# Performance work log

Hardware: AMD Instinct MI355X
Metric: run time of the kernel (lower is better)

Reference implementation:

```python
import jax, jax.numpy as jnp
import numpy as np

HEADS = 6
FILTERS = (16, 32, 64)
V_FEATS = 11
N_NODES = 30000
N_EDGES = 480000


def setup_inputs() -> dict:
    key = jax.random.key(0)
    ks = jax.random.split(key, 20)
    d = {}
    d["x_int"] = jax.random.normal(ks[0], (N_NODES, V_FEATS), jnp.float32)
    d["x_nh"] = jax.random.normal(ks[1], (N_NODES, V_FEATS), jnp.float32)
    d["ei_int"] = jax.random.randint(ks[2], (2, N_EDGES), 0, N_NODES, jnp.int32)
    d["ei_nh"] = jax.random.randint(ks[3], (2, N_EDGES), 0, N_NODES, jnp.int32)
    f_in = V_FEATS
    kidx = 4
    for i, f in enumerate(FILTERS, 1):
        s = 1.0 / np.sqrt(f_in)
        d[f"W{i}"] = (jax.random.normal(ks[kidx], (f_in, HEADS * f), jnp.float32) * s); kidx += 1
        sa = 1.0 / np.sqrt(f)
        d[f"a{i}s"] = (jax.random.normal(ks[kidx], (HEADS, f), jnp.float32) * sa); kidx += 1
        d[f"a{i}d"] = (jax.random.normal(ks[kidx], (HEADS, f), jnp.float32) * sa); kidx += 1
        f_in = HEADS * f
    d["Wd"] = jax.random.normal(ks[kidx], (2 * HEADS * FILTERS[-1], 1), jnp.float32) * 0.05
    d["bd"] = jnp.zeros((1,), jnp.float32)
    return d


def _gat_layer(h, src, dst, W, a_s, a_d):
    """One multi-head graph-attention (DGAT) layer, heads concatenated.
    h: [N, F_in]; W: [F_in, H*F_out]; a_s, a_d: [H, F_out]."""
    N = h.shape[0]
    H, Fo = a_s.shape
    z = (h @ W).reshape(N, H, Fo)                      # [N, H, Fo]
    e_src = jnp.einsum('nhf,hf->nh', z, a_s)           # [N, H]
    e_dst = jnp.einsum('nhf,hf->nh', z, a_d)
    e = jax.nn.leaky_relu(e_src[src] + e_dst[dst], 0.2)  # [E, H]
    # softmax over incoming edges of each destination node
    e_max = jax.ops.segment_max(e, dst, num_segments=N)  # [N, H] (-inf for empty)
    ex = jnp.exp(e - e_max[dst])
    denom = jax.ops.segment_sum(ex, dst, num_segments=N)
    alpha = ex / (denom[dst] + 1e-16)                   # [E, H]
    msg = z[src] * alpha[:, :, None]                    # [E, H, Fo]
    out = jax.ops.segment_sum(msg, dst, num_segments=N) # [N, H, Fo]
    return jax.nn.elu(out).reshape(N, H * Fo)


def reference(x_int, x_nh, W1, a1s, a1d, W2, a2s, a2d, W3, a3s, a3d, Wd, bd, ei_int, ei_nh):
    layers = [(W1, a1s, a1d), (W2, a2s, a2d), (W3, a3s, a3d)]

    def run(h, ei):
        src, dst = ei[0], ei[1]
        for (W, a_s, a_d) in layers:
            h = _gat_layer(h, src, dst, W, a_s, a_d)
        return h

    hi = run(x_int, ei_int)   # [N, 384]
    hn = run(x_nh, ei_nh)     # [N, 384]
    x = jnp.concatenate([hi, hn], axis=1)       # [N, 768]
    x = jnp.sum(x, axis=0).reshape(1, -1)       # [1, 768] sum pooling
    norm = jnp.maximum(jnp.linalg.norm(x, axis=1, keepdims=True), 1e-12)
    x = x / norm                                # F.normalize
    x = x @ Wd + bd                             # Dense, linear nonlin
    return jnp.squeeze(x, 1)                    # [1]
```

## Files before the change

### kernel.cpp

```cpp
#include <hip/hip_runtime.h>
#include <math.h>

#define N_NODES 30000
#define N_EDGES 480000
#define HEADS   6
#define NN2 (2 * N_NODES)
#define NE2 (2 * N_EDGES)

typedef __attribute__((ext_vector_type(8))) short bf16x8;
typedef __attribute__((ext_vector_type(4))) float f32x4;
typedef __attribute__((ext_vector_type(2))) float f32x2;
typedef __attribute__((ext_vector_type(4))) unsigned u32x4;

__device__ __forceinline__ unsigned short f2bf(float f) {
    unsigned u = __float_as_uint(f);
    u += 0x7fffu + ((u >> 16) & 1u);
    return (unsigned short)(u >> 16);
}

__global__ void gemm1_es_kernel(const float* __restrict__ x0, const float* __restrict__ x1,
                                const float* __restrict__ W, const float* __restrict__ a_s,
                                const float* __restrict__ a_d,
                                unsigned char* __restrict__ zf8b, float* __restrict__ es8,
                                float* __restrict__ ed8) {
    constexpr int K = 11, HF = 96, TM = 16, Fo = 16;
    __shared__ float hs[TM * K];
    const int m0 = blockIdx.x * TM;
    const float* h = (m0 < N_NODES) ? (x0 + (size_t)m0 * K)
                                    : (x1 + (size_t)(m0 - N_NODES) * K);
    const int j = blockIdx.y * 64 + threadIdx.x;
    for (int idx = threadIdx.x; idx < TM * K; idx += 64) hs[idx] = h[idx];
    __syncthreads();
    if (j >= HF) return;
    float acc[TM];
#pragma unroll
    for (int m = 0; m < TM; ++m) acc[m] = 0.f;
    for (int k = 0; k < K; ++k) {
        float w = W[k * HF + j];
#pragma unroll
        for (int m = 0; m < TM; ++m) acc[m] = fmaf(hs[m * K + k], w, acc[m]);
    }
    const float as_v = a_s[j];
    const float ad_v = a_d[j];
    const int hh = j >> 4;
    const int fo = j & 15;
#pragma unroll
    for (int m = 0; m < TM; ++m) {
        const int pk = __builtin_amdgcn_cvt_pk_fp8_f32(acc[m], acc[m], 0, false);
        zf8b[((size_t)hh * NN2 + (m0 + m)) * Fo + fo] = (unsigned char)pk;
    }
#pragma unroll
    for (int m = 0; m < TM; ++m) {
        float ep = acc[m] * as_v;
        float dp = acc[m] * ad_v;
#pragma unroll
        for (int d = 1; d < 16; d <<= 1) {
            ep += __shfl_xor(ep, d);
            dp += __shfl_xor(dp, d);
        }
        if ((threadIdx.x & 15) == 0) {
            es8[(size_t)(m0 + m) * 8 + hh] = ep;
            ed8[(size_t)(m0 + m) * 8 + hh] = dp;
        }
    }
}

__global__ void convert_wt_kernel(const float* __restrict__ W, unsigned short* __restrict__ Wt,
                                  int K, int HF) {
    const int idx = blockIdx.x * 256 + threadIdx.x;
    if (idx >= K * HF) return;
    const int k = idx / HF;
    const int n = idx - k * HF;
    Wt[n * K + k] = f2bf(W[idx]);
}

template <int K, int HF>
__global__ __launch_bounds__(256) void gemm_es_kernel(
        const unsigned short* __restrict__ hbf, const unsigned short* __restrict__ Wt,
        const float* __restrict__ a_s, const float* __restrict__ a_d,
        unsigned char* __restrict__ zf8b, float* __restrict__ es8,
        float* __restrict__ ed8) {
    constexpr int KSTEPS = K / 32;
    constexpr int Fo  = HF / HEADS;
    constexpr int TPH = Fo / 16;
    constexpr int NT  = HF / 16;
    constexpr int PAD = 8;
    constexpr int LROW = K + PAD;
    constexpr int NCH = 16 * K / 8;
    __shared__ unsigned short bl[16 * LROW];

    const int tid  = threadIdx.x;
    const int wid  = blockIdx.x * 4 + (tid >> 6);
    const bool active = wid < NN2 / 16;
    const int lane = tid & 63;
    const int r16  = lane & 15;
    const int quad = lane >> 4;
    const int m0 = active ? wid * 16 : 0;

    bf16x8 afrag[KSTEPS];
    const unsigned short* ap = hbf + (size_t)(m0 + r16) * K + quad * 8;
#pragma unroll
    for (int i = 0; i < KSTEPS; ++i) afrag[i] = *(const bf16x8*)(ap + i * 32);

    u32x4 st[2];
#pragma unroll
    for (int j = 0; j < 2; ++j) {
        const int c = tid + j * 256;
        if (c < NCH) st[j] = *(const u32x4*)(Wt + (size_t)c * 8);
    }

    float es_p[4] = {0.f, 0.f, 0.f, 0.f};
    float ed_p[4] = {0.f, 0.f, 0.f, 0.f};
    for (int t = 0; t < NT; ++t) {
        __syncthreads();
#pragma unroll
        for (int j = 0; j < 2; ++j) {
            const int c = tid + j * 256;
            if (c < NCH) {
                const int row = c / (K / 8);
                const int co  = c - row * (K / 8);
                *(u32x4*)(bl + row * LROW + co * 8) = st[j];
            }
        }
        if (t + 1 < NT) {
            const unsigned short* wp = Wt + (size_t)(t + 1) * 16 * K;
#pragma unroll
            for (int j = 0; j < 2; ++j) {
                const int c = tid + j * 256;
                if (c < NCH) st[j] = *(const u32x4*)(wp + (size_t)c * 8);
            }
        }
        __syncthreads();

        f32x4 acc = {0.f, 0.f, 0.f, 0.f};
        const unsigned short* bp = bl + r16 * LROW + quad * 8;
#pragma unroll
        for (int i = 0; i < KSTEPS; ++i) {
            const bf16x8 bfrag = *(const bf16x8*)(bp + i * 32);
            acc = __builtin_amdgcn_mfma_f32_16x16x32_bf16(afrag[i], bfrag, acc, 0, 0, 0);
        }
        const float as_v = a_s[t * 16 + r16];
        const float ad_v = a_d[t * 16 + r16];
        const int th = t / TPH;
        const int fo = (t % TPH) * 16 + r16;
        unsigned char* zp = zf8b + ((size_t)th * NN2 + (m0 + quad * 4)) * Fo + fo;
#pragma unroll
        for (int r = 0; r < 4; ++r) {
            const int pk = __builtin_amdgcn_cvt_pk_fp8_f32(acc[r], acc[r], 0, false);
            if (active) zp[(size_t)r * Fo] = (unsigned char)pk;
            es_p[r] = fmaf(acc[r], as_v, es_p[r]);
            ed_p[r] = fmaf(acc[r], ad_v, ed_p[r]);
        }
        if (((t + 1) % TPH) == 0) {
            const int h = t / TPH;
#pragma unroll
            for (int r = 0; r < 4; ++r) {
                float ep = es_p[r], dp = ed_p[r];
#pragma unroll
                for (int d = 1; d < 16; d <<= 1) {
                    ep += __shfl_xor(ep, d);
                    dp += __shfl_xor(dp, d);
                }
                if (active && r16 == 0) {
                    es8[(size_t)(m0 + quad * 4 + r) * 8 + h] = ep;
                    ed8[(size_t)(m0 + quad * 4 + r) * 8 + h] = dp;
                }
                es_p[r] = 0.f;
                ed_p[r] = 0.f;
            }
        }
    }
}

__global__ void zero_int_kernel(int* __restrict__ p, int n) {
    const int i = blockIdx.x * 256 + threadIdx.x;
    if (i < n) p[i] = 0;
}

__global__ void hist2_kernel(const int* __restrict__ ei0, const int* __restrict__ ei1,
                             int* __restrict__ cnt) {
    const int e = blockIdx.x * 256 + threadIdx.x;
    if (e >= NE2) return;
    const int g = e >= N_EDGES;
    const int* ei = g ? ei1 : ei0;
    const int e2 = e - g * N_EDGES;
    atomicAdd(&cnt[g * N_NODES + ei[N_EDGES + e2]], 1);
}

#define SCAN_NB ((NN2 + 1023) / 1024)
__global__ void scan1_kernel(int* tmp, int* __restrict__ bsum) {
    __shared__ int s[1024];
    const int t = threadIdx.x;
    const int gid = blockIdx.x * 1024 + t;
    const int v = (gid < NN2) ? tmp[gid] : 0;
    s[t] = v;
    __syncthreads();
    for (int d = 1; d < 1024; d <<= 1) {
        int x = (t >= d) ? s[t - d] : 0;
        __syncthreads();
        s[t] += x;
        __syncthreads();
    }
    tmp[gid] = s[t] - v;
    if (t == 1023) bsum[blockIdx.x] = s[1023];
}

__global__ void scan2_kernel(int* __restrict__ bsum, int* __restrict__ boff) {
    if (threadIdx.x == 0) {
        int a = 0;
        for (int i = 0; i < SCAN_NB; ++i) { boff[i] = a; a += bsum[i]; }
        boff[SCAN_NB] = a;
    }
}

__global__ void scan3_kernel(int* tmp, const int* __restrict__ boff,
                             int* __restrict__ off) {
    const int gid = blockIdx.x * 1024 + threadIdx.x;
    if (gid < NN2) {
        const int o = tmp[gid] + boff[gid >> 10];
        off[gid] = o;
        tmp[gid] = o;
    }
    if (gid == 0) off[NN2] = boff[SCAN_NB];
}

__global__ void scatter2_kernel(const int* __restrict__ ei0, const int* __restrict__ ei1,
                                int* __restrict__ cursor,
                                unsigned* __restrict__ csrp) {
    const int e = blockIdx.x * 256 + threadIdx.x;
    if (e >= NE2) return;
    const int g = e >= N_EDGES;
    const int* ei = g ? ei1 : ei0;
    const int e2 = e - g * N_EDGES;
    const int src = g * N_NODES + ei[e2];
    const int dst = g * N_NODES + ei[N_EDGES + e2];
    const int slot = atomicAdd(&cursor[dst], 1);
    csrp[slot] = ((unsigned)dst << 16) | (unsigned)src;
}

__global__ __launch_bounds__(256) void edgew_kernel(
        const unsigned* __restrict__ csrp,
        const float* __restrict__ es8, const float* __restrict__ ed8,
        unsigned* __restrict__ pA, unsigned* __restrict__ pB) {
    const int s = blockIdx.x * 256 + threadIdx.x;
    if (s >= NE2) return;
    const unsigned sd = csrp[s];
    const unsigned src = sd & 0xFFFFu;
    const unsigned dst = sd >> 16;
    const f32x4 ea = *(const f32x4*)(es8 + src * 8u);
    const f32x2 eb = *(const f32x2*)(es8 + src * 8u + 4);
    const f32x4 da = *(const f32x4*)(ed8 + dst * 8u);
    const f32x2 db = *(const f32x2*)(ed8 + dst * 8u + 4);
    float ev[6];
    ev[0] = ea.x + da.x; ev[1] = ea.y + da.y; ev[2] = ea.z + da.z;
    ev[3] = ea.w + da.w; ev[4] = eb.x + db.x; ev[5] = eb.y + db.y;
#pragma unroll
    for (int h = 0; h < 6; ++h) {
        float v = ev[h];
        v = fmaxf(v, 0.2f * v);
        const unsigned rec = ((unsigned)f2bf(__expf(v)) << 16) | src;
        unsigned* p = (h < 3) ? (pA + (size_t)h * NE2) : (pB + (size_t)(h - 3) * NE2);
        p[s] = rec;
    }
}

template <int HF, int GS, int MAIN, int G>
__global__ __launch_bounds__(256) void agg_sub_kernel(
        const int* __restrict__ off, const unsigned* __restrict__ ewA,
        const unsigned* __restrict__ ewB,
        const unsigned* __restrict__ zf8, unsigned short* __restrict__ outz) {
    constexpr int Fo  = HF / HEADS;
    constexpr int L   = Fo / 4;
    constexpr int EPI = GS / L;
    constexpr int GPW = 64 / GS;
    constexpr int NB  = 4 * GPW;
    constexpr int BPH = NN2 / NB;
    int h, blk;
    {
        const int r = blockIdx.x & 7, g = blockIdx.x >> 3;
        if (r < 6) {
            if (g >= MAIN) return;
            h = r; blk = g;
        } else {
            const int k = (r - 6) * G + g;
            if (k >= 6 * (BPH - MAIN)) return;
            h = k % 6; blk = MAIN + k / 6;
        }
    }
    const int wavid = threadIdx.x >> 6;
    const int lane  = threadIdx.x & 63;
    const int grp = lane / GS;
    const int lg  = lane - grp * GS;
    const int eo = lg / L;
    const int fp = lg - eo * L;
    const int n = blk * NB + wavid * GPW + grp;

    const int s0  = off[n];
    const int deg = off[n + 1] - s0;
    const unsigned* ewp = ((h < 3) ? (ewA + (size_t)h * NE2)
                                   : (ewB + (size_t)(h - 3) * NE2)) + s0;
    const unsigned* zh = zf8 + (size_t)h * ((size_t)NN2 * L);

    float a0 = 0.f, a1 = 0.f, a2 = 0.f, a3 = 0.f, lsum = 0.f;
    for (int ib = 0; ib < deg; ib += 4 * EPI) {
        unsigned rec[4];
#pragma unroll
        for (int k = 0; k < 4; ++k) {
            const int idx = ib + k * EPI + eo;
            rec[k] = ewp[idx < deg ? idx : 0];
        }
        unsigned zz[4];
#pragma unroll
        for (int k = 0; k < 4; ++k)
            zz[k] = zh[(rec[k] & 0xFFFFu) * (unsigned)L + (unsigned)fp];
#pragma unroll
        for (int k = 0; k < 4; ++k) {
            const int idx = ib + k * EPI + eo;
            float ww = __uint_as_float(rec[k] & 0xFFFF0000u);
            ww = (idx < deg) ? ww : 0.f;
            lsum += ww;
            const f32x2 lo = __builtin_amdgcn_cvt_pk_f32_fp8((int)zz[k], false);
            const f32x2 hi = __builtin_amdgcn_cvt_pk_f32_fp8((int)zz[k], true);
            a0 = fmaf(ww, lo.x, a0);
            a1 = fmaf(ww, lo.y, a1);
            a2 = fmaf(ww, hi.x, a2);
            a3 = fmaf(ww, hi.y, a3);
        }
    }
#pragma unroll
    for (int d = L; d < GS; d <<= 1) {
        a0 += __shfl_xor(a0, d);
        a1 += __shfl_xor(a1, d);
        a2 += __shfl_xor(a2, d);
        a3 += __shfl_xor(a3, d);
        lsum += __shfl_xor(lsum, d);
    }
    if (eo == 0) {
        const float inv = 1.f / (lsum + 1e-16f);
        float o0 = a0 * inv, o1 = a1 * inv, o2 = a2 * inv, o3 = a3 * inv;
        o0 = o0 > 0.f ? o0 : (__expf(o0) - 1.f);
        o1 = o1 > 0.f ? o1 : (__expf(o1) - 1.f);
        o2 = o2 > 0.f ? o2 : (__expf(o2) - 1.f);
        o3 = o3 > 0.f ? o3 : (__expf(o3) - 1.f);
        unsigned short* op = outz + (size_t)n * HF + h * Fo + 4 * fp;
        *(unsigned*)op       = (unsigned)f2bf(o0) | ((unsigned)f2bf(o1) << 16);
        *(unsigned*)(op + 2) = (unsigned)f2bf(o2) | ((unsigned)f2bf(o3) << 16);
    }
}

#define POOL_BLOCKS 3072
#define POOL_WAVES 2048
__global__ __launch_bounds__(256) void agg_pool_kernel(
        const int* __restrict__ off, const unsigned* __restrict__ ewA,
        const unsigned* __restrict__ ewB,
        const unsigned* __restrict__ zf8, float* __restrict__ pooled) {
    __shared__ float lds[128];
    int h, slot;
    {
        const int r = blockIdx.x & 7, g = blockIdx.x >> 3;
        if (r < 6) { h = r; slot = g; }
        else { h = g % 6; slot = 384 + (r - 6) * 64 + g / 6; }
    }
    const int wavid = threadIdx.x >> 6;
    const int ws    = slot * 4 + wavid;
    const int lane  = threadIdx.x & 63;
    const int c  = lane >> 2;
    const int fp = lane & 3;
    const unsigned* ewh = (h < 3) ? (ewA + (size_t)h * NE2)
                                  : (ewB + (size_t)(h - 3) * NE2);
    const u32x4* zq = (const u32x4*)(zf8 + (size_t)h * ((size_t)NN2 * 16));

    if (threadIdx.x < 128) lds[threadIdx.x] = 0.f;
    __syncthreads();

    float p0[16], p1[16];
#pragma unroll
    for (int j = 0; j < 16; ++j) { p0[j] = 0.f; p1[j] = 0.f; }

    for (int base = ws * 16; base < NN2; base += POOL_WAVES * 16) {
        const int n = base + c;
        const bool valid = n < NN2;
        int s0 = 0, deg = 0;
        if (valid) { s0 = off[n]; deg = off[n + 1] - s0; }
        int dmx = deg;
#pragma unroll
        for (int d = 4; d < 64; d <<= 1) {
            const int o = __shfl_xor(dmx, d);
            dmx = o > dmx ? o : dmx;
        }
        const unsigned* ewp = ewh + s0;
        float acc[16];
#pragma unroll
        for (int j = 0; j < 16; ++j) acc[j] = 0.f;
        float lsum = 0.f;
        for (int ib = 0; ib < dmx; ib += 4) {
            unsigned rec[4];
#pragma unroll
            for (int k = 0; k < 4; ++k) {
                const int idx = ib + k;
                rec[k] = ewp[idx < deg ? idx : 0];
            }
            u32x4 zz[4];
#pragma unroll
            for (int k = 0; k < 4; ++k)
                zz[k] = zq[(rec[k] & 0xFFFFu) * 4u + (unsigned)fp];
#pragma unroll
            for (int k = 0; k < 4; ++k) {
                float w = __uint_as_float(rec[k] & 0xFFFF0000u);
                w = ((ib + k) < deg) ? w : 0.f;
                lsum += w;
#pragma unroll
                for (int d = 0; d < 4; ++d) {
                    const f32x2 lo = __builtin_amdgcn_cvt_pk_f32_fp8((int)zz[k][d], false);
                    const f32x2 hi = __builtin_amdgcn_cvt_pk_f32_fp8((int)zz[k][d], true);
                    acc[4 * d + 0] = fmaf(w, lo.x, acc[4 * d + 0]);
                    acc[4 * d + 1] = fmaf(w, lo.y, acc[4 * d + 1]);
                    acc[4 * d + 2] = fmaf(w, hi.x, acc[4 * d + 2]);
                    acc[4 * d + 3] = fmaf(w, hi.y, acc[4 * d + 3]);
                }
            }
        }
        if (valid) {
            const float inv = 1.f / (lsum + 1e-16f);
            if (base < N_NODES) {
#pragma unroll
                for (int j = 0; j < 16; ++j) {
                    float o = acc[j] * inv;
                    o = o > 0.f ? o : (__expf(o) - 1.f);
                    p0[j] += o;
                }
            } else {
#pragma unroll
                for (int j = 0; j < 16; ++j) {
                    float o = acc[j] * inv;
                    o = o > 0.f ? o : (__expf(o) - 1.f);
                    p1[j] += o;
                }
            }
        }
    }
#pragma unroll
    for (int d = 4; d < 64; d <<= 1) {
#pragma unroll
        for (int j = 0; j < 16; ++j) {
            p0[j] += __shfl_xor(p0[j], d);
            p1[j] += __shfl_xor(p1[j], d);
        }
    }
    if (lane < 4) {
#pragma unroll
        for (int j = 0; j < 16; ++j) {
            atomicAdd(&lds[fp * 16 + j], p0[j]);
            atomicAdd(&lds[64 + fp * 16 + j], p1[j]);
        }
    }
    __syncthreads();
    if (threadIdx.x < 128) {
        const int g2 = threadIdx.x >> 6;
        const int f  = threadIdx.x & 63;
        atomicAdd(&pooled[g2 * 384 + h * 64 + f], lds[threadIdx.x]);
    }
}

__global__ void zero_pooled_kernel(float* __restrict__ p) {
    const int i = blockIdx.x * 256 + threadIdx.x;
    if (i < 768) p[i] = 0.f;
}

__global__ void final_kernel(const float* __restrict__ pooled, const float* __restrict__ Wd,
                             const float* __restrict__ bd, float* __restrict__ outp) {
    __shared__ float s_ss[256], s_dot[256];
    const int t = threadIdx.x;
    float ss = 0.f, dot = 0.f;
    for (int c = t; c < 768; c += 256) {
        const float v = pooled[c];
        ss  = fmaf(v, v, ss);
        dot = fmaf(v, Wd[c], dot);
    }
    s_ss[t] = ss; s_dot[t] = dot;
    __syncthreads();
    for (int off = 128; off > 0; off >>= 1) {
        if (t < off) { s_ss[t] += s_ss[t + off]; s_dot[t] += s_dot[t + off]; }
        __syncthreads();
    }
    if (t == 0) {
        const float norm = fmaxf(sqrtf(s_ss[0]), 1e-12f);
        outp[0] = s_dot[0] / norm + bd[0];
    }
}

extern "C" void kernel_launch(void* const* d_in, const int* in_sizes, int n_in,
                              void* d_out, int out_size, void* d_ws, size_t ws_size,
                              hipStream_t stream) {
    const float* x_int = (const float*)d_in[0];
    const float* x_nh  = (const float*)d_in[1];
    const int*   ei_int = (const int*)d_in[2];
    const int*   ei_nh  = (const int*)d_in[3];
    const float* W1  = (const float*)d_in[4];
    const float* a1s = (const float*)d_in[5];
    const float* a1d = (const float*)d_in[6];
    const float* W2  = (const float*)d_in[7];
    const float* a2s = (const float*)d_in[8];
    const float* a2d = (const float*)d_in[9];
    const float* W3  = (const float*)d_in[10];
    const float* a3s = (const float*)d_in[11];
    const float* a3d = (const float*)d_in[12];
    const float* Wd  = (const float*)d_in[13];
    const float* bd  = (const float*)d_in[14];
    float* out = (float*)d_out;

    unsigned short* hbf_a = (unsigned short*)d_ws;
    unsigned short* hbf_b = hbf_a + (size_t)NN2 * 96;
    unsigned short* wt2   = hbf_b + (size_t)NN2 * 192;
    unsigned short* wt3   = wt2   + (size_t)96 * 192;
    unsigned* zf8 = (unsigned*)(wt3 + (size_t)192 * 384);
    float* es8   = (float*)(zf8 + (size_t)NN2 * 96);
    float* ed8   = es8 + (size_t)NN2 * 8;
    float* pooled = ed8 + (size_t)NN2 * 8;
    int* tmp     = (int*)(pooled + 768);
    int* bsum    = tmp + SCAN_NB * 1024;
    int* boff    = bsum + SCAN_NB;
    int* off     = boff + SCAN_NB + 1;
    unsigned* csrp = (unsigned*)(off + NN2 + 1);
    unsigned char* zf8b = (unsigned char*)zf8;

    unsigned* ew13A = (unsigned*)hbf_b;
    unsigned* ew13B = ew13A + (size_t)3 * NE2;
    unsigned* ew2A  = (unsigned*)hbf_a;
    unsigned* ew2B  = zf8 + (size_t)NN2 * 48;

    zero_pooled_kernel<<<3, 256, 0, stream>>>(pooled);
    convert_wt_kernel<<<(96 * 192 + 255) / 256, 256, 0, stream>>>(W2, wt2, 96, 192);
    convert_wt_kernel<<<(192 * 384 + 255) / 256, 256, 0, stream>>>(W3, wt3, 192, 384);

    zero_int_kernel<<<(NN2 + 255) / 256, 256, 0, stream>>>(tmp, NN2);
    hist2_kernel<<<(NE2 + 255) / 256, 256, 0, stream>>>(ei_int, ei_nh, tmp);
    scan1_kernel<<<SCAN_NB, 1024, 0, stream>>>(tmp, bsum);
    scan2_kernel<<<1, 64, 0, stream>>>(bsum, boff);
    scan3_kernel<<<SCAN_NB, 1024, 0, stream>>>(tmp, boff, off);
    scatter2_kernel<<<(NE2 + 255) / 256, 256, 0, stream>>>(ei_int, ei_nh, tmp, csrp);

    const int mfma_blocks = (NN2 / 16 + 3) / 4;
    const int ew_blocks = (NE2 + 255) / 256;

    gemm1_es_kernel<<<dim3(NN2 / 16, 2), 64, 0, stream>>>(x_int, x_nh, W1, a1s, a1d, zf8b,
                                                          es8, ed8);
    edgew_kernel<<<ew_blocks, 256, 0, stream>>>(csrp, es8, ed8, ew13A, ew13B);
    agg_sub_kernel<96, 16, 2812, 2814><<<8 * 2814, 256, 0, stream>>>(off, ew13A, ew13B,
                                                                     zf8, hbf_a);
    gemm_es_kernel<96, 192><<<mfma_blocks, 256, 0, stream>>>(hbf_a, wt2, a2s, a2d, zf8b,
                                                             es8, ed8);
    edgew_kernel<<<ew_blocks, 256, 0, stream>>>(csrp, es8, ed8, ew2A, ew2B);
    agg_sub_kernel<192, 32, 5625, 5625><<<45000, 256, 0, stream>>>(off, ew2A, ew2B,
                                                                   zf8, hbf_b);
    gemm_es_kernel<192, 384><<<mfma_blocks, 256, 0, stream>>>(hbf_b, wt3, a3s, a3d, zf8b,
                                                              es8, ed8);
    edgew_kernel<<<ew_blocks, 256, 0, stream>>>(csrp, es8, ed8, ew13A, ew13B);
    agg_pool_kernel<<<POOL_BLOCKS, 256, 0, stream>>>(off, ew13A, ew13B, zf8, pooled);

    final_kernel<<<1, 256, 0, stream>>>(pooled, Wd, bd, out);
}
```

Before: 492.1 us.

## Sort nodes by in-degree so aggregation waves process similar-degree nodes

```diff
diff --git a/kernel.cpp b/kernel.cpp
--- a/kernel.cpp
+++ b/kernel.cpp
@@ -236,6 +236,39 @@
     const int dst = g * N_NODES + ei[N_EDGES + e2];
     const int slot = atomicAdd(&cursor[dst], 1);
     csrp[slot] = ((unsigned)dst << 16) | (unsigned)src;
+}
+
+__global__ void deghist_kernel(const int* __restrict__ off, int* __restrict__ dbuk) {
+    const int n = blockIdx.x * 256 + threadIdx.x;
+    if (n >= NN2) return;
+    const int deg = off[n + 1] - off[n];
+    const int b = deg < 511 ? deg : 511;
+    atomicAdd(&dbuk[(n >= N_NODES) * 512 + b], 1);
+}
+
+__global__ void degscan_kernel(int* __restrict__ dbuk) {
+    __shared__ int s[1024];
+    const int t = threadIdx.x;
+    const int v = dbuk[t];
+    s[t] = v;
+    __syncthreads();
+    for (int d = 1; d < 1024; d <<= 1) {
+        int x = (t >= d) ? s[t - d] : 0;
+        __syncthreads();
+        s[t] += x;
+        __syncthreads();
+    }
+    dbuk[t] = s[t] - v;
+}
+
+__global__ void degscatter_kernel(const int* __restrict__ off, int* __restrict__ dbuk,
+                                  unsigned short* __restrict__ sorted) {
+    const int n = blockIdx.x * 256 + threadIdx.x;
+    if (n >= NN2) return;
+    const int deg = off[n + 1] - off[n];
+    const int b = deg < 511 ? deg : 511;
+    const int pos = atomicAdd(&dbuk[(n >= N_NODES) * 512 + b], 1);
+    sorted[pos] = (unsigned short)n;
 }
 
 __global__ __launch_bounds__(256) void edgew_kernel(
@@ -266,8 +299,8 @@
 
 template <int HF, int GS, int MAIN, int G>
 __global__ __launch_bounds__(256) void agg_sub_kernel(
-        const int* __restrict__ off, const unsigned* __restrict__ ewA,
-        const unsigned* __restrict__ ewB,
+        const int* __restrict__ off, const unsigned short* __restrict__ sorted,
+        const unsigned* __restrict__ ewA, const unsigned* __restrict__ ewB,
         const unsigned* __restrict__ zf8, unsigned short* __restrict__ outz) {
     constexpr int Fo  = HF / HEADS;
     constexpr int L   = Fo / 4;
@@ -293,7 +326,8 @@
     const int lg  = lane - grp * GS;
     const int eo = lg / L;
     const int fp = lg - eo * L;
-    const int n = blk * NB + wavid * GPW + grp;
+    const int npos = blk * NB + wavid * GPW + grp;
+    const int n = sorted[npos];
 
     const int s0  = off[n];
     const int deg = off[n + 1] - s0;
@@ -351,8 +385,8 @@
 #define POOL_BLOCKS 3072
 #define POOL_WAVES 2048
 __global__ __launch_bounds__(256) void agg_pool_kernel(
-        const int* __restrict__ off, const unsigned* __restrict__ ewA,
-        const unsigned* __restrict__ ewB,
+        const int* __restrict__ off, const unsigned short* __restrict__ sorted,
+        const unsigned* __restrict__ ewA, const unsigned* __restrict__ ewB,
         const unsigned* __restrict__ zf8, float* __restrict__ pooled) {
     __shared__ float lds[128];
     int h, slot;
@@ -378,10 +412,10 @@
     for (int j = 0; j < 16; ++j) { p0[j] = 0.f; p1[j] = 0.f; }
 
     for (int base = ws * 16; base < NN2; base += POOL_WAVES * 16) {
-        const int n = base + c;
-        const bool valid = n < NN2;
-        int s0 = 0, deg = 0;
-        if (valid) { s0 = off[n]; deg = off[n + 1] - s0; }
+        const int npos = base + c;
+        const int n = sorted[npos];
+        const int s0  = off[n];
+        const int deg = off[n + 1] - s0;
         int dmx = deg;
 #pragma unroll
         for (int d = 4; d < 64; d <<= 1) {
@@ -420,7 +454,7 @@
                 }
             }
         }
-        if (valid) {
+        {
             const float inv = 1.f / (lsum + 1e-16f);
             if (base < N_NODES) {
 #pragma unroll
@@ -522,6 +556,7 @@
     int* boff    = bsum + SCAN_NB;
     int* off     = boff + SCAN_NB + 1;
     unsigned* csrp = (unsigned*)(off + NN2 + 1);
+    unsigned short* sorted = (unsigned short*)(csrp + NE2);
     unsigned char* zf8b = (unsigned char*)zf8;
 
     unsigned* ew13A = (unsigned*)hbf_b;
@@ -540,23 +575,29 @@
     scan3_kernel<<<SCAN_NB, 1024, 0, stream>>>(tmp, boff, off);
     scatter2_kernel<<<(NE2 + 255) / 256, 256, 0, stream>>>(ei_int, ei_nh, tmp, csrp);
 
+    zero_int_kernel<<<4, 256, 0, stream>>>(tmp, 1024);
+    deghist_kernel<<<(NN2 + 255) / 256, 256, 0, stream>>>(off, tmp);
+    degscan_kernel<<<1, 1024, 0, stream>>>(tmp);
+    degscatter_kernel<<<(NN2 + 255) / 256, 256, 0, stream>>>(off, tmp, sorted);
+
     const int mfma_blocks = (NN2 / 16 + 3) / 4;
     const int ew_blocks = (NE2 + 255) / 256;
 
     gemm1_es_kernel<<<dim3(NN2 / 16, 2), 64, 0, stream>>>(x_int, x_nh, W1, a1s, a1d, zf8b,
                                                           es8, ed8);
     edgew_kernel<<<ew_blocks, 256, 0, stream>>>(csrp, es8, ed8, ew13A, ew13B);
-    agg_sub_kernel<96, 16, 2812, 2814><<<8 * 2814, 256, 0, stream>>>(off, ew13A, ew13B,
-                                                                     zf8, hbf_a);
+    agg_sub_kernel<96, 16, 2812, 2814><<<8 * 2814, 256, 0, stream>>>(off, sorted, ew13A,
+                                                                     ew13B, zf8, hbf_a);
     gemm_es_kernel<96, 192><<<mfma_blocks, 256, 0, stream>>>(hbf_a, wt2, a2s, a2d, zf8b,
                                                              es8, ed8);
     edgew_kernel<<<ew_blocks, 256, 0, stream>>>(csrp, es8, ed8, ew2A, ew2B);
-    agg_sub_kernel<192, 32, 5625, 5625><<<45000, 256, 0, stream>>>(off, ew2A, ew2B,
-                                                                   zf8, hbf_b);
+    agg_sub_kernel<192, 32, 5625, 5625><<<45000, 256, 0, stream>>>(off, sorted, ew2A,
+                                                                   ew2B, zf8, hbf_b);
     gemm_es_kernel<192, 384><<<mfma_blocks, 256, 0, stream>>>(hbf_b, wt3, a3s, a3d, zf8b,
                                                               es8, ed8);
     edgew_kernel<<<ew_blocks, 256, 0, stream>>>(csrp, es8, ed8, ew13A, ew13B);
-    agg_pool_kernel<<<POOL_BLOCKS, 256, 0, stream>>>(off, ew13A, ew13B, zf8, pooled);
+    agg_pool_kernel<<<POOL_BLOCKS, 256, 0, stream>>>(off, sorted, ew13A, ew13B, zf8,
+                                                     pooled);
 
     final_kernel<<<1, 256, 0, stream>>>(pooled, Wd, bd, out);
 }
```

Measured after the change: 705.8 us. 1.43x slower.
